# Kernel tuning notes

Measured on AMD Instinct MI355X. Metric: run time of the kernel, lower is better.

Reference implementation:

```python
import jax, jax.numpy as jnp
import numpy as np

B, S, DIM, NQ, NKV = 2, 2048, 4096, 32, 8
HD = DIM // NQ  # 128


def _rope(t, fc):
    # t: [B,S,H,D]; fc: [S,D/2,2] = (cos,sin). Complex multiply on (even,odd) pairs.
    b, s, h, d = t.shape
    tp = t.astype(jnp.float32).reshape(b, s, h, d // 2, 2)
    c = fc[None, :, None, :, 0]
    sn = fc[None, :, None, :, 1]
    x0, x1 = tp[..., 0], tp[..., 1]
    rot = jnp.stack([x0 * c - x1 * sn, x0 * sn + x1 * c], axis=-1)
    return rot.reshape(b, s, h, d).astype(t.dtype)


def setup_inputs() -> dict:
    key = jax.random.key(0)
    ks = jax.random.split(key, 5)
    x = jax.random.normal(ks[0], (B, S, DIM), jnp.float32)
    wq = jax.random.normal(ks[1], (DIM, NQ * HD), jnp.float32) * 0.02
    wk = jax.random.normal(ks[2], (DIM, NKV * HD), jnp.float32) * 0.02
    wv = jax.random.normal(ks[3], (DIM, NKV * HD), jnp.float32) * 0.02
    wo = jax.random.normal(ks[4], (NQ * HD, DIM), jnp.float32) * 0.02
    # Llama RoPE frequencies for positions [0, S)
    inv_freq = 1.0 / (10000.0 ** (jnp.arange(0, HD, 2, dtype=jnp.float32) / HD))
    ang = jnp.arange(S, dtype=jnp.float32)[:, None] * inv_freq[None, :]  # [S, HD/2]
    freqs_cis = jnp.stack([jnp.cos(ang), jnp.sin(ang)], axis=-1)  # [S, HD/2, 2]
    cache_key = jnp.zeros((B, S, NKV, HD), jnp.float32)
    cache_value = jnp.zeros((B, S, NKV, HD), jnp.float32)
    return {"x": x, "start_pos": 0, "freqs_cis": freqs_cis, "wq": wq, "wk": wk,
            "wv": wv, "wo": wo, "cache_key": cache_key, "cache_value": cache_value}


def reference(x, start_pos, freqs_cis, wq, wk, wv, wo, cache_key, cache_value):
    b, s, dim = x.shape
    nkv, hd = cache_key.shape[2], cache_key.shape[3]
    nq = wq.shape[1] // hd
    n_rep = nq // nkv
    xq = (x @ wq).reshape(b, s, nq, hd)
    xk = (x @ wk).reshape(b, s, nkv, hd)
    xv = (x @ wv).reshape(b, s, nkv, hd)
    xq = _rope(xq, freqs_cis)
    xk = _rope(xk, freqs_cis)
    # KV-cache write then read of the valid prefix
    ck = jax.lax.dynamic_update_slice(cache_key, xk, (0, start_pos, 0, 0))
    cv = jax.lax.dynamic_update_slice(cache_value, xv, (0, start_pos, 0, 0))
    kv_len = start_pos + s
    k = ck[:, :kv_len]
    v = cv[:, :kv_len]
    # GQA: repeat_interleave kv heads to match q heads (as original materializes)
    keys = jnp.repeat(k, n_rep, axis=2)    # [B,K,NQ,HD]
    values = jnp.repeat(v, n_rep, axis=2)
    scale = 1.0 / jnp.sqrt(jnp.float32(hd))
    scores = jnp.einsum('bqhd,bkhd->bhqk', xq, keys) * scale  # [B,H,S,K]
    attn = jax.nn.softmax(scores, axis=-1)  # NOTE: no causal mask, as in source
    out = jnp.einsum('bhqk,bkhd->bqhd', attn, values).reshape(b, s, nq * hd)
    return out @ wo
```

## Files before the change

### kernel.cpp

```cpp
#include <hip/hip_runtime.h>
#include <stdint.h>


typedef __attribute__((ext_vector_type(8))) short short8;
typedef __attribute__((ext_vector_type(4))) float f32x4;
typedef __attribute__((ext_vector_type(16))) float f32x16;

#define DEVFN static __device__ __forceinline__

DEVFN ushort f2bf(float f) {
  uint32_t u = __builtin_bit_cast(uint32_t, f);
  u += 0x7fffu + ((u >> 16) & 1);
  return (ushort)(u >> 16);
}

DEVFN uint32_t pkbf(float a, float b) {
  return (uint32_t)f2bf(a) | ((uint32_t)f2bf(b) << 16);
}

DEVFN void gll16(const void* g, void* l) {
  __builtin_amdgcn_global_load_lds(
      (const __attribute__((address_space(1))) void*)g,
      (__attribute__((address_space(3))) void*)l, 16, 0, 0);
}

DEVFN float xhalf_max(float v) { return fmaxf(v, __shfl_xor(v, 32)); }
DEVFN float xhalf_add(float v) { return v + __shfl_xor(v, 32); }

DEVFN short8 mk_frag(uint32_t w0, uint32_t w1, uint32_t w2, uint32_t w3, int hi) {
  uint32_t x0 = __shfl_xor(w0, 32);
  uint32_t x1 = __shfl_xor(w1, 32);
  uint32_t x2 = __shfl_xor(w2, 32);
  uint32_t x3 = __shfl_xor(w3, 32);
  uint4 u;
  u.x = hi ? x2 : w0;
  u.y = hi ? x3 : w1;
  u.z = hi ? w2 : x0;
  u.w = hi ? w3 : x1;
  return __builtin_bit_cast(short8, u);
}

#define VMW(N) asm volatile("s_waitcnt vmcnt(" #N ")" ::: "memory")
#define SBAR()                        \
  do {                                \
    __builtin_amdgcn_s_barrier();     \
    __builtin_amdgcn_sched_barrier(0);\
  } while (0)

__global__ __launch_bounds__(256) void k_cvt(const float* __restrict__ src,
                                             ushort* __restrict__ dst, int n8) {
  int i = blockIdx.x * 256 + threadIdx.x;
  if (i >= n8) return;
  const float4* s4 = (const float4*)src + (size_t)i * 2;
  float4 a = s4[0], b = s4[1];
  uint4 o;
  o.x = (uint32_t)f2bf(a.x) | ((uint32_t)f2bf(a.y) << 16);
  o.y = (uint32_t)f2bf(a.z) | ((uint32_t)f2bf(a.w) << 16);
  o.z = (uint32_t)f2bf(b.x) | ((uint32_t)f2bf(b.y) << 16);
  o.w = (uint32_t)f2bf(b.z) | ((uint32_t)f2bf(b.w) << 16);
  ((uint4*)dst)[i] = o;
}

__global__ __launch_bounds__(256) void k_tr(const float* __restrict__ src,
                                            ushort* __restrict__ dst, int R, int C) {
  __shared__ float tile[64][65];
  const int c0 = blockIdx.x * 64, r0 = blockIdx.y * 64;
  const int t = threadIdx.x, rr = t >> 6, cc = t & 63;
#pragma unroll
  for (int i = 0; i < 16; ++i)
    tile[rr + i * 4][cc] = src[(size_t)(r0 + rr + i * 4) * C + c0 + cc];
  __syncthreads();
#pragma unroll
  for (int i = 0; i < 16; ++i)
    dst[(size_t)(c0 + rr + i * 4) * R + r0 + cc] = f2bf(tile[cc][rr + i * 4]);
}

template <int MODE>
__global__ __launch_bounds__(512, 2) void k_gemm8(
    const ushort* __restrict__ A, const ushort* __restrict__ Bp,
    const float* __restrict__ fcis, ushort* __restrict__ oQ,
    ushort* __restrict__ oK, ushort* __restrict__ oV, float* __restrict__ oC) {
  constexpr int K = 4096;
  constexpr int BN = MODE ? 256 : 192;
  constexpr int WN = BN / 4;
  constexpr int NF = WN / 16;
  constexpr int NBX = MODE ? 16 : 32;
  constexpr int ABUF = 16384;
  constexpr int BBUF = BN * 64;
  constexpr int NT = K / 32;

  __shared__ char smem[4 * ABUF + 4 * BBUF];
  char* AsL = smem;
  char* BsL = smem + 4 * ABUF;

  constexpr int nwg = NBX * 16;
  const int bid = blockIdx.x;
  const int wg = (bid & 7) * (nwg >> 3) + (bid >> 3);
  const int nb = wg % NBX, mb = wg / NBX;
  const int m0 = mb * 256, n0 = nb * BN;

  const int tid = threadIdx.x;
  const int w = tid >> 6, lane = tid & 63;
  const int gg = lane >> 4, rr = lane & 15;
  const int wm = w >> 2, wn = w & 3;

  const int l8 = lane >> 3, s7 = lane & 7;
  const int Ra0 = w * 8 + l8, Ra1 = 64 + Ra0;
  const int ea0 = s7 ^ (Ra0 & 7), ea1 = s7 ^ (Ra1 & 7);
  const ushort* agp0 = A + (size_t)(m0 + 2 * Ra0 + (ea0 >> 2)) * K + (ea0 & 3) * 8;
  const ushort* agp1 = A + (size_t)(m0 + 2 * Ra1 + (ea1 >> 2)) * K + (ea1 & 3) * 8;
  char* lda0 = AsL + w * 1024;
  char* lda1 = AsL + 8192 + w * 1024;

  const int Rb0 = w * 8 + l8;
  const int eb0 = s7 ^ (Rb0 & 7);
  const ushort* bgp0 = Bp + (size_t)(n0 + 2 * Rb0 + (eb0 >> 2)) * K + (eb0 & 3) * 8;
  char* ldb0 = BsL + w * 1024;
  const int Rb1 = MODE ? (64 + w * 8 + l8) : (64 + w * 4 + l8);
  const int eb1 = s7 ^ (Rb1 & 7);
  const ushort* bgp1 = Bp + (size_t)(n0 + 2 * Rb1 + (eb1 >> 2)) * K + (eb1 & 3) * 8;
  char* ldb1 = BsL + 8192 + (MODE ? w * 1024 : w * 512);

  auto STAGE_A = [&](int t) {
    const int bo = t & 3;
    const size_t ko = (size_t)t * 32;
    gll16(agp0 + ko, lda0 + bo * ABUF);
    gll16(agp1 + ko, lda1 + bo * ABUF);
  };
  auto STAGE_B = [&](int t) {
    const int bo = t & 3;
    const size_t ko = (size_t)t * 32;
    gll16(bgp0 + ko, ldb0 + bo * BBUF);
    if constexpr (MODE) {
      gll16(bgp1 + ko, ldb1 + bo * BBUF);
    } else {
      if (lane < 32) gll16(bgp1 + ko, ldb1 + bo * BBUF);
    }
  };

  int aoff[8], boff[NF];
#pragma unroll
  for (int mf = 0; mf < 8; ++mf) {
    const int m = wm * 128 + mf * 16 + rr;
    aoff[mf] = (m >> 1) * 128 + (((((m & 1) << 2) | gg) ^ ((m >> 1) & 7)) << 4);
  }
#pragma unroll
  for (int nf = 0; nf < NF; ++nf) {
    const int n = wn * WN + nf * 16 + rr;
    boff[nf] = (n >> 1) * 128 + (((((n & 1) << 2) | gg) ^ ((n >> 1) & 7)) << 4);
  }

  f32x4 acc[8][NF] = {};

  auto TILE = [&](int t, bool stg) {
    const int bo = t & 3;
    const char* Ab = AsL + bo * ABUF;
    const char* Bb = BsL + bo * BBUF;
    short8 bfr[NF], afr[4];
#pragma unroll
    for (int nf = 0; nf < NF; ++nf) bfr[nf] = *(const short8*)(Bb + boff[nf]);
#pragma unroll
    for (int i = 0; i < 4; ++i) afr[i] = *(const short8*)(Ab + aoff[i]);
    if (stg) STAGE_A(t + 3);
    SBAR();
    __builtin_amdgcn_s_setprio(1);
#pragma unroll
    for (int mi = 0; mi < 4; ++mi)
#pragma unroll
      for (int nf = 0; nf < NF; ++nf)
        acc[mi][nf] =
            __builtin_amdgcn_mfma_f32_16x16x32_bf16(afr[mi], bfr[nf], acc[mi][nf], 0, 0, 0);
    __builtin_amdgcn_s_setprio(0);
    SBAR();
#pragma unroll
    for (int i = 0; i < 4; ++i) afr[i] = *(const short8*)(Ab + aoff[4 + i]);
    if (stg) STAGE_B(t + 3);
    SBAR();
    __builtin_amdgcn_s_setprio(1);
#pragma unroll
    for (int mi = 0; mi < 4; ++mi)
#pragma unroll
      for (int nf = 0; nf < NF; ++nf)
        acc[4 + mi][nf] =
            __builtin_amdgcn_mfma_f32_16x16x32_bf16(afr[mi], bfr[nf], acc[4 + mi][nf], 0, 0, 0);
    __builtin_amdgcn_s_setprio(0);
  };

  STAGE_A(0); STAGE_B(0);
  STAGE_A(1); STAGE_B(1);
  STAGE_A(2); STAGE_B(2);
  VMW(8);
  SBAR();

  for (int t = 0; t < NT - 3; ++t) {
    TILE(t, true);
    VMW(8);
    SBAR();
  }
  TILE(NT - 3, false);
  VMW(4);
  SBAR();
  TILE(NT - 2, false);
  VMW(0);
  SBAR();
  TILE(NT - 1, false);

  if constexpr (MODE == 1) {
#pragma unroll
    for (int mf = 0; mf < 8; ++mf) {
      const int mbase = m0 + wm * 128 + mf * 16 + gg * 4;
#pragma unroll
      for (int nf = 0; nf < NF; ++nf) {
        const int n = n0 + wn * WN + nf * 16 + rr;
#pragma unroll
        for (int j = 0; j < 4; ++j)
          oC[(size_t)(mbase + j) * 4096 + n] = acc[mf][nf][j];
      }
    }
  } else {
    const int b = m0 >> 11;
#pragma unroll
    for (int mf = 0; mf < 8; ++mf) {
      const int mbase = m0 + wm * 128 + mf * 16 + gg * 4;
      const int s0 = mbase & 2047;
#pragma unroll
      for (int nf = 0; nf < NF; ++nf) {
        const int n = n0 + wn * WN + nf * 16 + rr;
        if (n < 5120) {
          const int d = n & 127, ii = d >> 1;
          const float sgn = (n & 1) ? 1.0f : -1.0f;
          const float qsc = (n < 4096) ? 0.12752364599362f : 1.0f;
          ushort res[4];
#pragma unroll
          for (int j = 0; j < 4; ++j) {
            const float2 cs = ((const float2*)fcis)[(size_t)(s0 + j) * 64 + ii];
            float v = acc[mf][nf][j];
            float pv = __shfl_xor(v, 1);
            res[j] = f2bf(qsc * (v * cs.x + sgn * pv * cs.y));
          }
          if (n < 4096) {
            ushort* dst = oQ + ((size_t)(b * 32 + (n >> 7)) * 2048 + s0) * 128 + d;
#pragma unroll
            for (int j = 0; j < 4; ++j) dst[j * 128] = res[j];
          } else {
            ushort* dst =
                oK + ((size_t)(b * 8 + ((n - 4096) >> 7)) * 2048 + s0) * 128 + d;
#pragma unroll
            for (int j = 0; j < 4; ++j) dst[j * 128] = res[j];
          }
        } else {
          const int n2 = n - 5120;
          ushort4 pk;
          pk.x = f2bf(acc[mf][nf][0]);
          pk.y = f2bf(acc[mf][nf][1]);
          pk.z = f2bf(acc[mf][nf][2]);
          pk.w = f2bf(acc[mf][nf][3]);
          *(ushort4*)&oV[((size_t)(b * 8 + (n2 >> 7)) * 128 + (n2 & 127)) * 2048 + s0] =
              pk;
        }
      }
    }
  }
}

__global__ __launch_bounds__(512, 2) void k_attn(const ushort* __restrict__ Qg,
                                                 const ushort* __restrict__ Kg,
                                                 const ushort* __restrict__ Vt,
                                                 ushort* __restrict__ Og) {
  __shared__ ushort Ks[2][64 * 128];
  __shared__ ushort Vs[2][64 * 128];
  __shared__ float sml[8][32];

  const int bh = blockIdx.x, qt = blockIdx.y;
  const int b = bh >> 5, h = bh & 31, hk = h >> 2;
  const int t = threadIdx.x, w = t >> 6, lane = t & 63;
  const int ln31 = lane & 31, hi = lane >> 5;
  const int q0 = qt * 256;

  short8 qf[8];
  {
    const size_t qbase = ((size_t)bh * 2048 + q0 + w * 32 + ln31) * 128;
#pragma unroll
    for (int tt = 0; tt < 8; ++tt)
      qf[tt] = *(const short8*)&Qg[qbase + tt * 16 + hi * 8];
  }
  const size_t kgb = (size_t)(b * 8 + hk) * 2048 * 128;
  const size_t vgb = (size_t)(b * 8 + hk) * 128 * 2048;

  const int srow = t >> 3;
  const int ssl = (t & 7) * 2;
  const int s0 = ssl ^ (srow & 15);
  const int vd = 2 * (t >> 3) + ((t & 7) >> 2);
  const int vkl = (t & 3) * 16;
  const ushort* kgp = Kg + kgb + (size_t)srow * 128 + ssl * 8;
  const ushort* vgp = Vt + vgb + (size_t)vd * 2048 + vkl;

  uint4 rk0, rk1, rv0, rv1;
  auto LOAD = [&](int k0) {
    const uint4* kp = (const uint4*)(kgp + (size_t)k0 * 128);
    rk0 = kp[0];
    rk1 = kp[1];
    const uint4* vp = (const uint4*)(vgp + k0);
    rv0 = vp[0];
    rv1 = vp[1];
  };
  auto STORE = [&](int buf) {
    char* kd = (char*)Ks[buf] + srow * 256;
    *(uint4*)(kd + (s0 << 4)) = rk0;
    *(uint4*)(kd + ((s0 ^ 1) << 4)) = rk1;
    char* vdd = (char*)Vs[buf] + srow * 256;
    *(uint4*)(vdd + (s0 << 4)) = rv0;
    *(uint4*)(vdd + ((s0 ^ 1) << 4)) = rv1;
  };

  f32x16 ov[4] = {};
  float m_run = -1e30f, l_run = 0.f;

  const int mk = ln31 & 15;
  const int krb0 = ln31 * 256, krb1 = krb0 + 8192;
  const int vrb = (ln31 >> 1) * 256;
  const int vsp = (ln31 & 1) * 8 + hi;
  const int mv = ln31 >> 1;

  LOAD(0);
  STORE(0);
  __syncthreads();

  for (int tile = 0; tile < 32; ++tile) {
    const int cur = tile & 1;
    if (tile < 31) LOAD((tile + 1) * 64);

    const char* Kc = (const char*)Ks[cur];
    f32x16 p0 = {}, p1 = {};
#pragma unroll
    for (int tt = 0; tt < 8; ++tt) {
      const int sl = ((tt * 2 + hi) ^ mk) << 4;
      short8 ka0 = *(const short8*)(Kc + krb0 + sl);
      short8 ka1 = *(const short8*)(Kc + krb1 + sl);
      p0 = __builtin_amdgcn_mfma_f32_32x32x16_bf16(ka0, qf[tt], p0, 0, 0, 0);
      p1 = __builtin_amdgcn_mfma_f32_32x32x16_bf16(ka1, qf[tt], p1, 0, 0, 0);
    }

    float vmx = p0[0];
#pragma unroll
    for (int i = 1; i < 16; ++i) vmx = fmaxf(vmx, p0[i]);
#pragma unroll
    for (int i = 0; i < 16; ++i) vmx = fmaxf(vmx, p1[i]);
    const float pmax = xhalf_max(vmx);
    if (!__all(pmax <= m_run + 8.0f)) {
      const float mnew = fmaxf(m_run, pmax);
      const float al = exp2f(m_run - mnew);
      m_run = mnew;
      l_run *= al;
      sml[w][ln31] = al;
      const float4 a0 = *(const float4*)&sml[w][hi * 4];
      const float4 a1 = *(const float4*)&sml[w][8 + hi * 4];
      const float4 a2 = *(const float4*)&sml[w][16 + hi * 4];
      const float4 a3 = *(const float4*)&sml[w][24 + hi * 4];
      const float aa[16] = {a0.x, a0.y, a0.z, a0.w, a1.x, a1.y, a1.z, a1.w,
                            a2.x, a2.y, a2.z, a2.w, a3.x, a3.y, a3.z, a3.w};
#pragma unroll
      for (int i = 0; i < 16; ++i) {
        ov[0][i] *= aa[i]; ov[1][i] *= aa[i];
        ov[2][i] *= aa[i]; ov[3][i] *= aa[i];
      }
    }
#pragma unroll
    for (int i = 0; i < 16; ++i) p0[i] = exp2f(p0[i] - m_run);
#pragma unroll
    for (int i = 0; i < 16; ++i) p1[i] = exp2f(p1[i] - m_run);
    float ls = 0.f;
#pragma unroll
    for (int i = 0; i < 16; ++i) ls += p0[i] + p1[i];
    l_run += xhalf_add(ls);

    short8 pa[4];
    pa[0] = mk_frag(pkbf(p0[0], p0[1]), pkbf(p0[2], p0[3]),
                    pkbf(p0[4], p0[5]), pkbf(p0[6], p0[7]), hi);
    pa[1] = mk_frag(pkbf(p0[8], p0[9]), pkbf(p0[10], p0[11]),
                    pkbf(p0[12], p0[13]), pkbf(p0[14], p0[15]), hi);
    pa[2] = mk_frag(pkbf(p1[0], p1[1]), pkbf(p1[2], p1[3]),
                    pkbf(p1[4], p1[5]), pkbf(p1[6], p1[7]), hi);
    pa[3] = mk_frag(pkbf(p1[8], p1[9]), pkbf(p1[10], p1[11]),
                    pkbf(p1[12], p1[13]), pkbf(p1[14], p1[15]), hi);

    const char* Vc = (const char*)Vs[cur];
#pragma unroll
    for (int db = 0; db < 4; ++db) {
      const int rb = vrb + db * 4096;
#pragma unroll
      for (int ks = 0; ks < 4; ++ks) {
        const int sl = ((vsp + ks * 2) ^ mv) << 4;
        short8 bv = *(const short8*)(Vc + rb + sl);
        ov[db] = __builtin_amdgcn_mfma_f32_32x32x16_bf16(pa[ks], bv, ov[db], 0, 0, 0);
      }
    }

    if (tile < 31) STORE(cur ^ 1);
    __syncthreads();
  }

  sml[w][ln31] = l_run;
  const float4 l0 = *(const float4*)&sml[w][hi * 4];
  const float4 l1 = *(const float4*)&sml[w][8 + hi * 4];
  const float4 l2 = *(const float4*)&sml[w][16 + hi * 4];
  const float4 l3 = *(const float4*)&sml[w][24 + hi * 4];
  const float inv[16] = {1.f / l0.x, 1.f / l0.y, 1.f / l0.z, 1.f / l0.w,
                         1.f / l1.x, 1.f / l1.y, 1.f / l1.z, 1.f / l1.w,
                         1.f / l2.x, 1.f / l2.y, 1.f / l2.z, 1.f / l2.w,
                         1.f / l3.x, 1.f / l3.y, 1.f / l3.z, 1.f / l3.w};
  const int qb0 = q0 + w * 32 + hi * 4;
#pragma unroll
  for (int rg = 0; rg < 4; ++rg)
#pragma unroll
    for (int j = 0; j < 4; ++j) {
      const int sq = qb0 + rg * 8 + j;
      const size_t orow = ((size_t)(b * 2048 + sq)) * 4096 + h * 128 + ln31;
#pragma unroll
      for (int db = 0; db < 4; ++db)
        Og[orow + db * 32] = f2bf(ov[db][rg * 4 + j] * inv[rg * 4 + j]);
    }
}

extern "C" void kernel_launch(void* const* d_in, const int* in_sizes, int n_in,
                              void* d_out, int out_size, void* d_ws, size_t ws_size,
                              hipStream_t stream) {
  const float* x = (const float*)d_in[0];
  const float* fcis = (const float*)d_in[2];
  const float* wq = (const float*)d_in[3];
  const float* wk = (const float*)d_in[4];
  const float* wv = (const float*)d_in[5];
  const float* wo = (const float*)d_in[6];
  float* out = (float*)d_out;

  char* ws = (char*)d_ws;
  ushort* xb  = (ushort*)(ws);
  ushort* wsT = (ushort*)(ws + 33554432u);
  ushort* qb  = (ushort*)(ws + 83886080u);
  ushort* kb  = (ushort*)(ws + 117440512u);
  ushort* vbT = (ushort*)(ws + 125829120u);
  ushort* woT = xb;
  ushort* ao  = wsT;

  k_cvt<<<8192, 256, 0, stream>>>(x, xb, 2097152);
  k_tr<<<dim3(64, 64), 256, 0, stream>>>(wq, wsT, 4096, 4096);
  k_tr<<<dim3(16, 64), 256, 0, stream>>>(wk, wsT + (size_t)4096 * 4096, 4096, 1024);
  k_tr<<<dim3(16, 64), 256, 0, stream>>>(wv, wsT + (size_t)5120 * 4096, 4096, 1024);
  k_gemm8<0><<<512, 512, 0, stream>>>(xb, wsT, fcis, qb, kb, vbT, nullptr);
  k_tr<<<dim3(64, 64), 256, 0, stream>>>(wo, woT, 4096, 4096);
  k_attn<<<dim3(64, 8), 512, 0, stream>>>(qb, kb, vbT, ao);
  k_gemm8<1><<<256, 512, 0, stream>>>(ao, woT, nullptr, nullptr, nullptr, nullptr,
                                      out);
}
```

Before: 588.4 us.

## Software-pipeline GEMM LDS fragment reads with double-buffered registers and fewer barriers

Restructures the GEMM main loop so the LDS fragment reads for the next tile go into alternate register sets while MFMAs run on the current tile. This cuts the number of workgroup barriers per tile from three to one. The loop is manually unrolled by two with a hardcoded trip count of 128 tiles, and MODE 1 reloads B fragments each iteration. The extra fragment registers may raise register pressure, and the fixed tile count assumes K=4096.

```diff
diff --git a/kernel.cpp b/kernel.cpp
--- a/kernel.cpp
+++ b/kernel.cpp
@@ -41,11 +41,6 @@
 }
 
 #define VMW(N) asm volatile("s_waitcnt vmcnt(" #N ")" ::: "memory")
-#define SBAR()                        \
-  do {                                \
-    __builtin_amdgcn_s_barrier();     \
-    __builtin_amdgcn_sched_barrier(0);\
-  } while (0)
 
 __global__ __launch_bounds__(256) void k_cvt(const float* __restrict__ src,
                                              ushort* __restrict__ dst, int n8) {
@@ -151,59 +146,72 @@
   }
 
   f32x4 acc[8][NF] = {};
-
-  auto TILE = [&](int t, bool stg) {
-    const int bo = t & 3;
-    const char* Ab = AsL + bo * ABUF;
-    const char* Bb = BsL + bo * BBUF;
-    short8 bfr[NF], afr[4];
-#pragma unroll
-    for (int nf = 0; nf < NF; ++nf) bfr[nf] = *(const short8*)(Bb + boff[nf]);
-#pragma unroll
-    for (int i = 0; i < 4; ++i) afr[i] = *(const short8*)(Ab + aoff[i]);
-    if (stg) STAGE_A(t + 3);
-    SBAR();
-    __builtin_amdgcn_s_setprio(1);
+  short8 X0[4], X1[4], Y0[4], Y1[4];
+  short8 Bc0[NF], Bc1[NF];
+
+  auto RD_A = [&](int tt, short8* d, int h) {
+    const char* Ab = AsL + (tt & 3) * ABUF;
+#pragma unroll
+    for (int i = 0; i < 4; ++i) d[i] = *(const short8*)(Ab + aoff[h * 4 + i]);
+  };
+  auto RD_B = [&](int tt, short8* d) {
+    const char* Bb = BsL + (tt & 3) * BBUF;
+#pragma unroll
+    for (int nf = 0; nf < NF; ++nf) d[nf] = *(const short8*)(Bb + boff[nf]);
+  };
+  auto MFMA_H = [&](short8* a, short8* bfr, int h) {
 #pragma unroll
     for (int mi = 0; mi < 4; ++mi)
 #pragma unroll
       for (int nf = 0; nf < NF; ++nf)
-        acc[mi][nf] =
-            __builtin_amdgcn_mfma_f32_16x16x32_bf16(afr[mi], bfr[nf], acc[mi][nf], 0, 0, 0);
-    __builtin_amdgcn_s_setprio(0);
-    SBAR();
-#pragma unroll
-    for (int i = 0; i < 4; ++i) afr[i] = *(const short8*)(Ab + aoff[4 + i]);
-    if (stg) STAGE_B(t + 3);
-    SBAR();
-    __builtin_amdgcn_s_setprio(1);
-#pragma unroll
-    for (int mi = 0; mi < 4; ++mi)
-#pragma unroll
-      for (int nf = 0; nf < NF; ++nf)
-        acc[4 + mi][nf] =
-            __builtin_amdgcn_mfma_f32_16x16x32_bf16(afr[mi], bfr[nf], acc[4 + mi][nf], 0, 0, 0);
-    __builtin_amdgcn_s_setprio(0);
-  };
+        acc[h + mi][nf] = __builtin_amdgcn_mfma_f32_16x16x32_bf16(
+            a[mi], bfr[nf], acc[h + mi][nf], 0, 0, 0);
+  };
+
+#define GITER(T, cA0, cA1, cB, nA0, nA1, nB, STG, VN)                \
+  do {                                                               \
+    if constexpr (MODE == 1) RD_B((T), Bc0); \
+    RD_A((T) + 1, nA0, 0);                                           \
+    if constexpr (MODE == 0) RD_B((T) + 1, nB);                      \
+    __builtin_amdgcn_sched_barrier(0);                               \
+    __builtin_amdgcn_s_setprio(1);                                   \
+    MFMA_H(cA0, (MODE == 1) ? Bc0 : cB, 0);                          \
+    __builtin_amdgcn_s_setprio(0);                                   \
+    RD_A((T) + 1, nA1, 1);                                           \
+    if (STG) { STAGE_A((T) + 3); STAGE_B((T) + 3); }                 \
+    __builtin_amdgcn_sched_barrier(0);                               \
+    __builtin_amdgcn_s_setprio(1);                                   \
+    MFMA_H(cA1, (MODE == 1) ? Bc0 : cB, 4);                          \
+    __builtin_amdgcn_s_setprio(0);                                   \
+    VMW(VN);                                                         \
+    __builtin_amdgcn_s_barrier();                                    \
+    __builtin_amdgcn_sched_barrier(0);                               \
+  } while (0)
 
   STAGE_A(0); STAGE_B(0);
   STAGE_A(1); STAGE_B(1);
   STAGE_A(2); STAGE_B(2);
-  VMW(8);
-  SBAR();
-
-  for (int t = 0; t < NT - 3; ++t) {
-    TILE(t, true);
-    VMW(8);
-    SBAR();
-  }
-  TILE(NT - 3, false);
   VMW(4);
-  SBAR();
-  TILE(NT - 2, false);
-  VMW(0);
-  SBAR();
-  TILE(NT - 1, false);
+  __builtin_amdgcn_s_barrier();
+  __builtin_amdgcn_sched_barrier(0);
+  RD_A(0, X0, 0);
+  RD_A(0, X1, 1);
+  if constexpr (MODE == 0) RD_B(0, Bc0);
+
+  for (int tp = 0; tp < 62; ++tp) {
+    const int T = 2 * tp;
+    GITER(T, X0, X1, Bc0, Y0, Y1, Bc1, true, 4);
+    GITER(T + 1, Y0, Y1, Bc1, X0, X1, Bc0, true, 4);
+  }
+  GITER(124, X0, X1, Bc0, Y0, Y1, Bc1, true, 4);
+  GITER(125, Y0, Y1, Bc1, X0, X1, Bc0, false, 0);
+  GITER(126, X0, X1, Bc0, Y0, Y1, Bc1, false, 0);
+  if constexpr (MODE == 1) RD_B(127, Bc0);
+  __builtin_amdgcn_s_setprio(1);
+  MFMA_H(Y0, (MODE == 1) ? Bc0 : Bc1, 0);
+  MFMA_H(Y1, (MODE == 1) ? Bc0 : Bc1, 4);
+  __builtin_amdgcn_s_setprio(0);
+#undef GITER
 
   if constexpr (MODE == 1) {
 #pragma unroll
```

After: 570.4 us. 3.1% less time.
